# Kernel tuning notes

Hardware: AMD Instinct MI355X
Metric: run time of the kernel (lower is better)

Reference implementation:

```python
import jax, jax.numpy as jnp
import numpy as np

PATCH_PERCENTAGE = 0.5
THRESHOLD = 0.3
GAUSSIAN_STD = 0.25


def _center_of_gravity(line_drawing):
    # line_drawing: [B, 1, H, W]
    B, _, H, W = line_drawing.shape
    y = jnp.linspace(0.0, 1.0, H).reshape(1, 1, H, 1)
    x = jnp.linspace(0.0, 1.0, W).reshape(1, 1, 1, W)
    total = line_drawing.sum(axis=(2, 3)) + 1e-6          # [B, 1]
    cog_y = (line_drawing * y).sum(axis=(2, 3)) / total    # [B, 1]
    cog_x = (line_drawing * x).sum(axis=(2, 3)) / total    # [B, 1]
    return jnp.concatenate([cog_y, cog_x], axis=1)         # [B, 2] (y, x)


def _gaussian_weights(side, centers):
    # centers: [B, 2]; returns [B, side*side]
    lin = jnp.linspace(0.0, 1.0, side)
    gy, gx = jnp.meshgrid(lin, lin, indexing='ij')
    coords = jnp.stack([gy.ravel(), gx.ravel()], axis=1)   # [N, 2]
    d2 = ((coords[None, :, :] - centers[:, None, :]) ** 2).sum(-1)  # [B, N]
    return jnp.exp(-d2 / (2.0 * GAUSSIAN_STD ** 2))


def _selection_indices(scores, line_drawing, k):
    B, N = scores.shape
    side = int(np.sqrt(N))
    centers = _center_of_gravity(line_drawing)
    weights = _gaussian_weights(side, centers)
    weighted = scores * weights                            # [B, N]

    above = weighted > THRESHOLD                           # [B, N]
    count = above.sum(axis=1)                              # [B]
    idx = jnp.arange(N)

    # ascending above-threshold indices first (matches torch.where order)
    sort_key = jnp.where(above, idx[None, :], N + idx[None, :])
    above_sorted = jnp.argsort(sort_key, axis=1)[:, :k]    # [B, k]

    # top-k over below-threshold scores (above ones masked to -inf)
    masked = jnp.where(above, -jnp.inf, weighted)
    _, topk_masked = jax.lax.top_k(masked, k)              # [B, k]
    _, topk_all = jax.lax.top_k(weighted, k)               # [B, k]

    pos = jnp.arange(k)[None, :]                           # [1, k]
    shift = jnp.clip(pos - count[:, None], 0, k - 1)
    remaining = jnp.take_along_axis(topk_masked, shift, axis=1)
    combined = jnp.where(pos < count[:, None], above_sorted, remaining)

    use_topk = (count >= k) | (count == 0)                 # [B]
    return jnp.where(use_topk[:, None], topk_all, combined)


def setup_inputs() -> dict:
    key = jax.random.key(0)
    k1, k2, k3, k4 = jax.random.split(key, 4)
    B, N, D, HW = 64, 784, 768, 448
    return {
        'magno_patches': jax.random.normal(k1, (B, N, D), dtype=jnp.float32),
        'vit_positional_embedding': jax.random.normal(k2, (1, N + 1, D), dtype=jnp.float32),
        'scores': jax.random.uniform(k3, (B, N), dtype=jnp.float32),
        'line_drawing': jax.random.uniform(k4, (B, 1, HW, HW), dtype=jnp.float32),
    }


def reference(magno_patches, vit_positional_embedding, scores, line_drawing):
    B, N, D = magno_patches.shape
    k = int(N * PATCH_PERCENTAGE)
    sel = _selection_indices(scores, line_drawing, k)       # [B, k] int32

    sel_patches = jnp.take_along_axis(magno_patches, sel[:, :, None], axis=1)
    pos_embed = jnp.broadcast_to(vit_positional_embedding[:, 1:, :], (B, N, D))
    sel_pos = jnp.take_along_axis(pos_embed, sel[:, :, None], axis=1)
    return sel_patches + sel_pos
```

## Files before the change

kernel.cpp:

```cpp
#include <hip/hip_runtime.h>
#include <math.h>

#define BATCH 64
#define NPATCH 784
#define DIM 768
#define KSEL 392
#define SIDE 28
#define HWDIM 448
#define NPIX (HWDIM*HWDIM)
#define PARTS 49
#define PIX_PER_PART (NPIX/PARTS)
#define GSPLIT 4
#define IPB 196

typedef float f4v __attribute__((ext_vector_type(4)));
typedef unsigned long long u64;

__global__ __launch_bounds__(256) void cog_partial(const float* __restrict__ ld,
                                                   double* __restrict__ part) {
    const int blk = blockIdx.x;
    const int b = blk / PARTS;
    const int p = blk % PARTS;
    const int t = threadIdx.x;

    __shared__ alignas(16) float lin[HWDIM];
    for (int e = t; e < HWDIM; e += 256) lin[e] = (float)((double)e / 447.0);
    __syncthreads();

    const float* base = ld + (size_t)b * NPIX + (size_t)p * PIX_PER_PART;
    double s = 0.0, sy = 0.0, sx = 0.0;

    #pragma unroll
    for (int r = 0; r < 4; ++r) {
        const int f4 = r * 256 + t;
        const int pix = p * PIX_PER_PART + f4 * 4;
        const f4v v = reinterpret_cast<const f4v*>(base)[f4];
        const int i = pix / HWDIM;
        const int j = pix - i * HWDIM;
        const float yf = lin[i];
        const f4v xq = *reinterpret_cast<const f4v*>(&lin[j]);
        s  += (double)v.x + (double)v.y + (double)v.z + (double)v.w;
        sy += (double)__fmul_rn(v.x, yf) + (double)__fmul_rn(v.y, yf)
            + (double)__fmul_rn(v.z, yf) + (double)__fmul_rn(v.w, yf);
        sx += (double)__fmul_rn(v.x, xq.x) + (double)__fmul_rn(v.y, xq.y)
            + (double)__fmul_rn(v.z, xq.z) + (double)__fmul_rn(v.w, xq.w);
    }

    __shared__ double red[3 * 256];
    red[t] = s; red[256 + t] = sy; red[512 + t] = sx;
    __syncthreads();
    for (int off = 128; off > 0; off >>= 1) {
        if (t < off) {
            red[t]       += red[t + off];
            red[256 + t] += red[256 + t + off];
            red[512 + t] += red[512 + t + off];
        }
        __syncthreads();
    }
    if (t == 0) {
        double* dst = part + (size_t)(b * PARTS + p) * 3;
        dst[0] = red[0]; dst[1] = red[256]; dst[2] = red[512];
    }
}

__global__ __launch_bounds__(256) void select_k(const float* __restrict__ scores,
                                                const double* __restrict__ part,
                                                int* __restrict__ sel) {
    const int blk = blockIdx.x;
    const int b = blk / GSPLIT;
    const int g = blk % GSPLIT;
    const int t = threadIdx.x;
    const int wid = t >> 6;
    const int lane = t & 63;

    __shared__ double sd[3][64];
    __shared__ float scog[2];
    __shared__ alignas(16) u64 skey[NPATCH];
    __shared__ u64 ajm[16];

    if (t < 64) {
        if (t < PARTS) {
            const double* src = part + (size_t)(b * PARTS + t) * 3;
            sd[0][t] = src[0]; sd[1][t] = src[1]; sd[2][t] = src[2];
        } else {
            sd[0][t] = 0.0; sd[1][t] = 0.0; sd[2][t] = 0.0;
        }
    }
    __syncthreads();
    for (int off = 32; off > 0; off >>= 1) {
        if (t < off) {
            sd[0][t] += sd[0][t + off];
            sd[1][t] += sd[1][t + off];
            sd[2][t] += sd[2][t + off];
        }
        __syncthreads();
    }
    if (t == 0) {
        const float total = __fadd_rn((float)sd[0][0], 1e-6f);
        scog[0] = __fdiv_rn((float)sd[1][0], total);
        scog[1] = __fdiv_rn((float)sd[2][0], total);
    }
    __syncthreads();
    const float cy = scog[0];
    const float cx = scog[1];

    #pragma unroll
    for (int pass = 0; pass < 4; ++pass) {
        const int n = pass * 256 + t;
        const bool valid = n < NPATCH;
        float wt = 0.0f;
        if (valid) {
            const int r = n / SIDE;
            const int c = n - r * SIDE;
            const float gy = (float)((double)r / 27.0);
            const float gx = (float)((double)c / 27.0);
            const float dy = gy - cy;
            const float dx = gx - cx;
            const float dy2 = __fmul_rn(dy, dy);
            const float dx2 = __fmul_rn(dx, dx);
            const float d2 = __fadd_rn(dy2, dx2);
            const float w = (float)exp((double)(-8.0f * d2));
            wt = __fmul_rn(scores[(size_t)b * NPATCH + n], w);
            skey[n] = ((u64)__float_as_uint(wt) << 10) | (u64)(1023 - n);
        }
        const u64 m = __ballot(valid && (wt > 0.3f));
        if (lane == 0) ajm[pass * 4 + wid] = m;
    }
    __syncthreads();

    const int i = g * IPB + t;
    if (t < IPB) {
        const u64 ki = skey[i];
        int r0 = 0, r1 = 0, r2 = 0, r3 = 0;
        #pragma unroll 4
        for (int j = 0; j < NPATCH; j += 4) {
            r0 += skey[j + 0] > ki;
            r1 += skey[j + 1] > ki;
            r2 += skey[j + 2] > ki;
            r3 += skey[j + 3] > ki;
        }
        const int r_all = (r0 + r1) + (r2 + r3);

        int count = 0;
        #pragma unroll
        for (int q = 0; q < 16; ++q) count += __popcll(ajm[q]);

        const int qi = i >> 6;
        const bool above_i = (ajm[qi] >> (u64)(i & 63)) & 1ull;
        int r_pre = 0;
        for (int q = 0; q < qi; ++q) r_pre += __popcll(ajm[q]);
        r_pre += __popcll(ajm[qi] & ((1ull << (u64)(i & 63)) - 1ull));

        const bool use_topk = (count == 0) || (count >= KSEL);
        const int dst = (!use_topk && above_i) ? r_pre : r_all;
        if (dst < KSEL) sel[(size_t)b * KSEL + dst] = i;
    }
}

__global__ __launch_bounds__(256) void gather_add(const float* __restrict__ magno,
                                                  const float* __restrict__ pos,
                                                  const int* __restrict__ sel,
                                                  float* __restrict__ out) {
    const int wid = threadIdx.x >> 6;
    const int lane = threadIdx.x & 63;
    const int row = blockIdx.x * 4 + wid;
    const int b = row / KSEL;
    const int s = sel[row];

    const f4v* src = reinterpret_cast<const f4v*>(magno + ((size_t)b * NPATCH + s) * DIM);
    const f4v* pp  = reinterpret_cast<const f4v*>(pos + (size_t)(s + 1) * DIM);
    f4v* dst = reinterpret_cast<f4v*>(out + (size_t)row * DIM);

    const f4v a0 = src[lane], a1 = src[64 + lane], a2 = src[128 + lane];
    const f4v p0 = pp[lane],  p1 = pp[64 + lane],  p2 = pp[128 + lane];
    dst[lane]       = a0 + p0;
    dst[64 + lane]  = a1 + p1;
    dst[128 + lane] = a2 + p2;
}

extern "C" void kernel_launch(void* const* d_in, const int* in_sizes, int n_in,
                              void* d_out, int out_size, void* d_ws, size_t ws_size,
                              hipStream_t stream) {
    const float* magno  = (const float*)d_in[0];
    const float* vit    = (const float*)d_in[1];
    const float* scores = (const float*)d_in[2];
    const float* ld     = (const float*)d_in[3];
    float* out = (float*)d_out;

    double* partials = (double*)d_ws;
    int*    sel = (int*)((char*)d_ws + (size_t)BATCH * PARTS * 3 * sizeof(double));

    cog_partial<<<dim3(BATCH * PARTS), dim3(256), 0, stream>>>(ld, partials);
    select_k<<<dim3(BATCH * GSPLIT), dim3(256), 0, stream>>>(scores, partials, sel);
    gather_add<<<dim3(BATCH * KSEL / 4), dim3(256), 0, stream>>>(magno, vit, sel, out);
}
```

Baseline: 54.11 us.

## Fuse center-of-gravity and selection kernels via per-batch atomic arrival counter

Merges the partial center-of-gravity reduction and the top-k selection into one kernel. The last GSPLIT blocks to arrive for each batch, identified by an atomic counter, spin-wait until all partials are written and then run the selection. This removes one kernel launch and the gap between launches, but adds a memset, atomics, spin-waiting and higher shared-memory use per block. The gather kernel now writes its output with nontemporal stores.

```diff
diff --git a/kernel.cpp b/kernel.cpp
--- a/kernel.cpp
+++ b/kernel.cpp
@@ -16,68 +16,77 @@
 typedef float f4v __attribute__((ext_vector_type(4)));
 typedef unsigned long long u64;
 
-__global__ __launch_bounds__(256) void cog_partial(const float* __restrict__ ld,
-                                                   double* __restrict__ part) {
+__global__ __launch_bounds__(256) void cog_select(
+        const float* __restrict__ ld,
+        const float* __restrict__ scores,
+        double* __restrict__ part,
+        unsigned* __restrict__ cnt,
+        int* __restrict__ sel) {
     const int blk = blockIdx.x;
     const int b = blk / PARTS;
     const int p = blk % PARTS;
     const int t = threadIdx.x;
+    const int wid = t >> 6;
+    const int lane = t & 63;
 
     __shared__ alignas(16) float lin[HWDIM];
     for (int e = t; e < HWDIM; e += 256) lin[e] = (float)((double)e / 447.0);
     __syncthreads();
 
-    const float* base = ld + (size_t)b * NPIX + (size_t)p * PIX_PER_PART;
-    double s = 0.0, sy = 0.0, sx = 0.0;
-
-    #pragma unroll
-    for (int r = 0; r < 4; ++r) {
-        const int f4 = r * 256 + t;
-        const int pix = p * PIX_PER_PART + f4 * 4;
-        const f4v v = reinterpret_cast<const f4v*>(base)[f4];
-        const int i = pix / HWDIM;
-        const int j = pix - i * HWDIM;
-        const float yf = lin[i];
-        const f4v xq = *reinterpret_cast<const f4v*>(&lin[j]);
-        s  += (double)v.x + (double)v.y + (double)v.z + (double)v.w;
-        sy += (double)__fmul_rn(v.x, yf) + (double)__fmul_rn(v.y, yf)
-            + (double)__fmul_rn(v.z, yf) + (double)__fmul_rn(v.w, yf);
-        sx += (double)__fmul_rn(v.x, xq.x) + (double)__fmul_rn(v.y, xq.y)
-            + (double)__fmul_rn(v.z, xq.z) + (double)__fmul_rn(v.w, xq.w);
-    }
-
-    __shared__ double red[3 * 256];
-    red[t] = s; red[256 + t] = sy; red[512 + t] = sx;
-    __syncthreads();
-    for (int off = 128; off > 0; off >>= 1) {
-        if (t < off) {
-            red[t]       += red[t + off];
-            red[256 + t] += red[256 + t + off];
-            red[512 + t] += red[512 + t + off];
-        }
+    {
+        const float* base = ld + (size_t)b * NPIX + (size_t)p * PIX_PER_PART;
+        double s = 0.0, sy = 0.0, sx = 0.0;
+        #pragma unroll
+        for (int r = 0; r < 4; ++r) {
+            const int f4 = r * 256 + t;
+            const int pix = p * PIX_PER_PART + f4 * 4;
+            const f4v v = reinterpret_cast<const f4v*>(base)[f4];
+            const int i = pix / HWDIM;
+            const int j = pix - i * HWDIM;
+            const float yf = lin[i];
+            const f4v xq = *reinterpret_cast<const f4v*>(&lin[j]);
+            s  += (double)v.x + (double)v.y + (double)v.z + (double)v.w;
+            sy += (double)__fmul_rn(v.x, yf) + (double)__fmul_rn(v.y, yf)
+                + (double)__fmul_rn(v.z, yf) + (double)__fmul_rn(v.w, yf);
+            sx += (double)__fmul_rn(v.x, xq.x) + (double)__fmul_rn(v.y, xq.y)
+                + (double)__fmul_rn(v.z, xq.z) + (double)__fmul_rn(v.w, xq.w);
+        }
+
+        __shared__ double red[3 * 256];
+        red[t] = s; red[256 + t] = sy; red[512 + t] = sx;
         __syncthreads();
-    }
+        for (int off = 128; off > 0; off >>= 1) {
+            if (t < off) {
+                red[t]       += red[t + off];
+                red[256 + t] += red[256 + t + off];
+                red[512 + t] += red[512 + t + off];
+            }
+            __syncthreads();
+        }
+        if (t == 0) {
+            double* dst = part + (size_t)(b * PARTS + p) * 3;
+            dst[0] = red[0]; dst[1] = red[256]; dst[2] = red[512];
+        }
+    }
+
+    __shared__ int sg;
     if (t == 0) {
-        double* dst = part + (size_t)(b * PARTS + p) * 3;
-        dst[0] = red[0]; dst[1] = red[256]; dst[2] = red[512];
-    }
-}
-
-__global__ __launch_bounds__(256) void select_k(const float* __restrict__ scores,
-                                                const double* __restrict__ part,
-                                                int* __restrict__ sel) {
-    const int blk = blockIdx.x;
-    const int b = blk / GSPLIT;
-    const int g = blk % GSPLIT;
-    const int t = threadIdx.x;
-    const int wid = t >> 6;
-    const int lane = t & 63;
+        const unsigned prev = __hip_atomic_fetch_add(&cnt[b], 1u,
+                                  __ATOMIC_ACQ_REL, __HIP_MEMORY_SCOPE_AGENT);
+        sg = (int)prev - (PARTS - GSPLIT);
+    }
+    __syncthreads();
+    const int g = sg;
+    if (g < 0) return;
+
+    while (__hip_atomic_load(&cnt[b], __ATOMIC_ACQUIRE, __HIP_MEMORY_SCOPE_AGENT)
+           < (unsigned)PARTS) {
+        __builtin_amdgcn_s_sleep(8);
+    }
+    __syncthreads();
 
     __shared__ double sd[3][64];
     __shared__ float scog[2];
-    __shared__ alignas(16) u64 skey[NPATCH];
-    __shared__ u64 ajm[16];
-
     if (t < 64) {
         if (t < PARTS) {
             const double* src = part + (size_t)(b * PARTS + t) * 3;
@@ -104,6 +113,8 @@
     const float cy = scog[0];
     const float cx = scog[1];
 
+    __shared__ alignas(16) u64 skey[NPATCH];
+    __shared__ u64 ajm[16];
     #pragma unroll
     for (int pass = 0; pass < 4; ++pass) {
         const int n = pass * 256 + t;
@@ -173,9 +184,9 @@
 
     const f4v a0 = src[lane], a1 = src[64 + lane], a2 = src[128 + lane];
     const f4v p0 = pp[lane],  p1 = pp[64 + lane],  p2 = pp[128 + lane];
-    dst[lane]       = a0 + p0;
-    dst[64 + lane]  = a1 + p1;
-    dst[128 + lane] = a2 + p2;
+    __builtin_nontemporal_store(a0 + p0, dst + lane);
+    __builtin_nontemporal_store(a1 + p1, dst + 64 + lane);
+    __builtin_nontemporal_store(a2 + p2, dst + 128 + lane);
 }
 
 extern "C" void kernel_launch(void* const* d_in, const int* in_sizes, int n_in,
@@ -187,10 +198,11 @@
     const float* ld     = (const float*)d_in[3];
     float* out = (float*)d_out;
 
-    double* partials = (double*)d_ws;
-    int*    sel = (int*)((char*)d_ws + (size_t)BATCH * PARTS * 3 * sizeof(double));
-
-    cog_partial<<<dim3(BATCH * PARTS), dim3(256), 0, stream>>>(ld, partials);
-    select_k<<<dim3(BATCH * GSPLIT), dim3(256), 0, stream>>>(scores, partials, sel);
+    double*   partials = (double*)d_ws;
+    int*      sel = (int*)((char*)d_ws + (size_t)BATCH * PARTS * 3 * sizeof(double));
+    unsigned* cnt = (unsigned*)((char*)sel + (size_t)BATCH * KSEL * sizeof(int));
+
+    hipMemsetAsync(cnt, 0, BATCH * sizeof(unsigned), stream);
+    cog_select<<<dim3(BATCH * PARTS), dim3(256), 0, stream>>>(ld, scores, partials, cnt, sel);
     gather_add<<<dim3(BATCH * KSEL / 4), dim3(256), 0, stream>>>(magno, vit, sel, out);
 }
```

Measured after the change: 169.8 us. 214% more time.
